# Kernel tuning notes

Measured on AMD Instinct MI355X. Metric: run time of the kernel, lower is better.

Reference implementation:

```python
import jax, jax.numpy as jnp
import numpy as np

B, SQ, SKV, D, H = 2, 2048, 2048, 1024, 16
HD = D // H  # 64
ROPE_BASE = 10000.0


def setup_inputs() -> dict:
    key = jax.random.key(0)
    ks = jax.random.split(key, 6)
    s = 1.0 / np.sqrt(D)  # keep activations well-scaled
    return {
        "x_q": jax.random.normal(ks[0], (B, SQ, D), jnp.float32),
        "x_kv": jax.random.normal(ks[1], (B, SKV, D), jnp.float32),
        "wq": jax.random.normal(ks[2], (D, D), jnp.float32) * s,
        "bq": jnp.zeros((D,), jnp.float32),
        "wk": jax.random.normal(ks[3], (D, D), jnp.float32) * s,
        "bk": jnp.zeros((D,), jnp.float32),
        "wv": jax.random.normal(ks[4], (D, D), jnp.float32) * s,
        "bv": jnp.zeros((D,), jnp.float32),
        "wo": jax.random.normal(ks[5], (D, D), jnp.float32) * s,
        "bo": jnp.zeros((D,), jnp.float32),
    }


def _rope_interleaved(x):
    # x: [B, S, H, HD]; sequential positions starting at 0 (GPT-NeoX style)
    s, hd = x.shape[1], x.shape[-1]
    dim = hd // 2
    freqs = jnp.exp(-jnp.arange(dim, dtype=x.dtype) * jnp.log(jnp.asarray(ROPE_BASE, x.dtype)) / dim)
    ang = jnp.arange(s, dtype=x.dtype)[:, None] * freqs[None, :]  # [S, dim]
    cos = jnp.cos(ang)[None, :, None, :]
    sin = jnp.sin(ang)[None, :, None, :]
    xe, xo = x[..., ::2], x[..., 1::2]
    re = xe * cos - xo * sin
    ro = xe * sin + xo * cos
    return jnp.stack([re, ro], axis=-1).reshape(x.shape)


def reference(x_q, x_kv, wq, bq, wk, bk, wv, bv, wo, bo):
    b, sq, _ = x_q.shape
    skv = x_kv.shape[1]
    q = (jnp.einsum("bsd,ed->bse", x_q, wq) + bq).reshape(b, sq, H, HD)
    k = (jnp.einsum("bsd,ed->bse", x_kv, wk) + bk).reshape(b, skv, H, HD)
    v = (jnp.einsum("bsd,ed->bse", x_kv, wv) + bv).reshape(b, skv, H, HD)
    q = _rope_interleaved(q)
    k = _rope_interleaved(k)
    scores = jnp.einsum("bqhd,bkhd->bhqk", q, k) / jnp.sqrt(jnp.asarray(HD, q.dtype))
    attn = jax.nn.softmax(scores, axis=-1)
    ctx = jnp.einsum("bhqk,bkhd->bqhd", attn, v).reshape(b, sq, D)
    return jnp.einsum("bsd,ed->bse", ctx, wo) + bo
```

## Files before the change

kernel.cpp:

```cpp
#include <hip/hip_runtime.h>
#include <cstdint>

typedef __attribute__((ext_vector_type(8))) short bf16x8;
typedef __attribute__((ext_vector_type(4))) float f32x4;
typedef __attribute__((ext_vector_type(4))) unsigned int u32x4;

#define DEV static __device__ __forceinline__

DEV unsigned short f2bf(float f) {
  unsigned int u = __builtin_bit_cast(unsigned int, f);
  u += 0x7FFFu + ((u >> 16) & 1u);
  return (unsigned short)(u >> 16);
}
#if __has_builtin(__builtin_amdgcn_cvt_pk_bf16_f32)
DEV unsigned int pkbf(float a, float b) {
  auto v = __builtin_amdgcn_cvt_pk_bf16_f32(a, b);
  return __builtin_bit_cast(unsigned int, v);
}
#else
DEV unsigned int pkbf(float a, float b) {
  return (unsigned int)f2bf(a) | ((unsigned int)f2bf(b) << 16);
}
#endif
#if __has_builtin(__builtin_amdgcn_exp2f)
#define EXP2(x) __builtin_amdgcn_exp2f(x)
#else
#define EXP2(x) exp2f(x)
#endif
DEV float bfl(unsigned int u) { return __builtin_bit_cast(float, u << 16); }
DEV float bfh(unsigned int u) { return __builtin_bit_cast(float, u & 0xFFFF0000u); }

DEV void async_copy16(const unsigned short* g, unsigned short* l) {
  __builtin_amdgcn_global_load_lds(
      (const __attribute__((address_space(1))) unsigned int*)(uintptr_t)g,
      (__attribute__((address_space(3))) unsigned int*)(uintptr_t)l,
      16, 0, 0);
}

#if __has_builtin(__builtin_amdgcn_permlane32_swap) && \
    __has_builtin(__builtin_amdgcn_permlane16_swap)
DEV void pswap(unsigned a, unsigned b, unsigned& w0, unsigned& w2, int lane) {
  (void)lane;
  auto pq = __builtin_amdgcn_permlane32_swap((int)a, (int)b, false, false);
  auto wz = __builtin_amdgcn_permlane16_swap(pq[0], pq[1], false, false);
  w0 = (unsigned)wz[0];
  w2 = (unsigned)wz[1];
}
#else
DEV void pswap(unsigned a, unsigned b, unsigned& w0, unsigned& w2, int lane) {
  int q = lane >> 4, l = lane & 15;
  int src0 = ((q & 1) << 5) + l;
  int a0 = __shfl((int)a, src0), b0 = __shfl((int)b, src0);
  int a2 = __shfl((int)a, src0 + 16), b2 = __shfl((int)b, src0 + 16);
  w0 = (unsigned)(q < 2 ? a0 : b0);
  w2 = (unsigned)(q < 2 ? a2 : b2);
}
#endif

__global__ __launch_bounds__(256) void cvt8(
    const float* __restrict__ w0, const float* __restrict__ w1,
    const float* __restrict__ w2, const float* __restrict__ w3,
    const float* __restrict__ x0, const float* __restrict__ x1,
    unsigned short* __restrict__ wsb, unsigned short* __restrict__ xb)
{
  int id = blockIdx.x * 256 + threadIdx.x;
  const float* src;
  unsigned short* dp;
  int off;
  if (id < (1 << 20)) {
    int m = id >> 18;
    off = (id & 0x3FFFF) << 2;
    src = m == 0 ? w0 : m == 1 ? w1 : m == 2 ? w2 : w3;
    dp = wsb + (((size_t)m) << 20) + off;
  } else {
    int id2 = id - (1 << 20);
    int m = id2 >> 20;
    off = (id2 & 0xFFFFF) << 2;
    src = m ? x1 : x0;
    dp = xb + (((size_t)m) << 22) + off;
  }
  float4 v = *(const float4*)(src + off);
  uint2 o;
  o.x = pkbf(v.x, v.y);
  o.y = pkbf(v.z, v.w);
  *(uint2*)dp = o;
}

__global__ __launch_bounds__(256) void gemm_qkv_bf(
    const unsigned short* __restrict__ xqb,
    const unsigned short* __restrict__ xkvb,
    const unsigned short* __restrict__ wbase,
    const float* __restrict__ bq, const float* __restrict__ bk,
    const float* __restrict__ bv,
    unsigned short* __restrict__ outq, unsigned short* __restrict__ outk,
    unsigned short* __restrict__ outvT)
{
  constexpr int K = 1024;
  __shared__ unsigned short As[2][128 * 32];
  __shared__ unsigned short Bs[2][128 * 32];
  const int z = blockIdx.z;
  const unsigned short* X = (z == 0) ? xqb : xkvb;
  const unsigned short* Wb = wbase + (((size_t)z) << 20);
  const float* bias = (z == 0) ? bq : (z == 1) ? bk : bv;

  const int tid = threadIdx.x;
  const int mBase = blockIdx.y * 128, nBase = blockIdx.x * 128;
  const int wave = tid >> 6, lane = tid & 63;
  const int quad = lane >> 4, l16 = lane & 15;
  const int wm = (wave >> 1) << 6, wn = (wave & 1) << 6;

  const int L0 = tid, L1 = 256 + tid;
  const int r0 = L0 >> 2, c0 = ((L0 & 3) ^ (r0 & 3)) << 3;
  const int r1 = L1 >> 2, c1 = ((L1 & 3) ^ (r1 & 3)) << 3;

  f32x4 acc[4][4] = {};

  async_copy16(X + (size_t)(mBase + r0) * K + c0, &As[0][L0 * 8]);
  async_copy16(X + (size_t)(mBase + r1) * K + c1, &As[0][L1 * 8]);
  async_copy16(Wb + (size_t)(nBase + r0) * K + c0, &Bs[0][L0 * 8]);
  async_copy16(Wb + (size_t)(nBase + r1) * K + c1, &Bs[0][L1 * 8]);
  __syncthreads();

  const int sw = (quad ^ (l16 & 3)) << 3;
  for (int it = 0; it < 32; ++it) {
    const int cur = it & 1;
    if (it < 31) {
      const int k0 = (it + 1) * 32;
      async_copy16(X + (size_t)(mBase + r0) * K + k0 + c0, &As[cur ^ 1][L0 * 8]);
      async_copy16(X + (size_t)(mBase + r1) * K + k0 + c1, &As[cur ^ 1][L1 * 8]);
      async_copy16(Wb + (size_t)(nBase + r0) * K + k0 + c0, &Bs[cur ^ 1][L0 * 8]);
      async_copy16(Wb + (size_t)(nBase + r1) * K + k0 + c1, &Bs[cur ^ 1][L1 * 8]);
    }
    bf16x8 af[4], bff[4];
#pragma unroll
    for (int t = 0; t < 4; ++t) {
      af[t]  = *(const bf16x8*)&As[cur][(wm + t * 16 + l16) * 32 + sw];
      bff[t] = *(const bf16x8*)&Bs[cur][(wn + t * 16 + l16) * 32 + sw];
    }
#pragma unroll
    for (int mt = 0; mt < 4; ++mt)
#pragma unroll
      for (int nt = 0; nt < 4; ++nt)
        acc[mt][nt] = __builtin_amdgcn_mfma_f32_16x16x32_bf16(af[mt], bff[nt], acc[mt][nt], 0, 0, 0);
    __syncthreads();
  }

  if (z < 2) {
    unsigned short* out = z ? outk : outq;
    const float qs = z ? 1.0f : 0.18033688011112042f;
    const int sBlk = (mBase & 2047) + wm + quad * 4;
#pragma unroll
    for (int nt = 0; nt < 4; ++nt) {
      int n = nBase + wn + nt * 16 + l16;
      float bv2 = bias[n];
      int h = n >> 6, hd = n & 63;
      int i = hd >> 1;
      int parity = n & 1;
      float f = exp2f(-(float)i * 0.4152410118609203f);
      float sf, cf;
      sincosf(f, &sf, &cf);
#pragma unroll
      for (int mt = 0; mt < 4; ++mt) {
        float ang = (float)(sBlk + mt * 16) * f;
        float s, c;
        sincosf(ang, &s, &c);
#pragma unroll
        for (int j = 0; j < 4; ++j) {
          float v = acc[mt][nt][j] + bv2;
          float pv = __shfl_xor(v, 1);
          float ce = c * qs;
          float se = (parity ? s : -s) * qs;
          float outv = v * ce + pv * se;
          int m = mBase + wm + mt * 16 + quad * 4 + j;
          int b = m >> 11, sv = m & 2047;
          out[(((size_t)(b * 16 + h) * 2048 + sv) << 6) + hd] = f2bf(outv);
          float c2 = c * cf - s * sf;
          s = s * cf + c * sf;
          c = c2;
        }
      }
    }
  } else {
#pragma unroll
    for (int nt = 0; nt < 4; ++nt) {
      int n = nBase + wn + nt * 16 + l16;
      float bv2 = bias[n];
      int h = n >> 6, hd = n & 63;
#pragma unroll
      for (int mt = 0; mt < 4; ++mt) {
        int m0 = mBase + wm + mt * 16 + quad * 4;
        int b = m0 >> 11, s = m0 & 2047;
        uint2 o;
        o.x = pkbf(acc[mt][nt][0] + bv2, acc[mt][nt][1] + bv2);
        o.y = pkbf(acc[mt][nt][2] + bv2, acc[mt][nt][3] + bv2);
        *(uint2*)&outvT[(((size_t)(b * 16 + h) * 64 + hd) << 11) + s] = o;
      }
    }
  }
}

__global__ __launch_bounds__(256) void attn_v7(
    const unsigned short* __restrict__ Qg,
    const unsigned short* __restrict__ Kg,
    const unsigned short* __restrict__ VT,
    unsigned short* __restrict__ Opart,
    float* __restrict__ lbuf)
{
  __shared__ unsigned short Ks[2][64 * 64];
  __shared__ unsigned short Vs[2][64 * 64];
  const int tid = threadIdx.x, wave = tid >> 6, lane = tid & 63;
  const int quad = lane >> 4, l16 = lane & 15;
  const int bh = blockIdx.x & 31;
  const int qt = (blockIdx.x >> 5) & 15;
  const int kvs = blockIdx.x >> 9;
  const int q0 = qt * 128 + wave * 32;
  const unsigned short* Qb = Qg + ((size_t)bh << 17);
  const unsigned short* Kb = Kg + ((size_t)bh << 17);
  const unsigned short* Vb = VT + ((size_t)bh << 17);

  const int L0 = tid, L1 = 256 + tid;
  const int r0 = L0 >> 3, r1 = L1 >> 3;
  const int c0 = ((L0 & 7) ^ (r0 & 7)) << 3;
  const int c1 = ((L1 & 7) ^ (r1 & 7)) << 3;

  bf16x8 qf[2][2];
#pragma unroll
  for (int mq = 0; mq < 2; ++mq)
#pragma unroll
    for (int kd = 0; kd < 2; ++kd)
      qf[mq][kd] = *(const bf16x8*)(Qb + (size_t)(q0 + mq * 16 + l16) * 64 + kd * 32 + quad * 8);

  f32x4 oacc[4][2] = {};
  float lacc[2] = { 0.f, 0.f };

  const int kvbeg = kvs << 10;
  const int swz = l16 & 7;

  {
    const int kv0 = kvbeg;
    async_copy16(Kb + (size_t)(kv0 + r0) * 64 + c0, &Ks[0][L0 * 8]);
    async_copy16(Kb + (size_t)(kv0 + r1) * 64 + c1, &Ks[0][L1 * 8]);
    async_copy16(Vb + (size_t)r0 * 2048 + kv0 + c0, &Vs[0][L0 * 8]);
    async_copy16(Vb + (size_t)r1 * 2048 + kv0 + c1, &Vs[0][L1 * 8]);
  }
  __syncthreads();

  for (int t = 0; t < 16; ++t) {
    const int cur = t & 1;
    if (t < 15) {
      const int kv0 = kvbeg + (t + 1) * 64;
      unsigned short* Kn = Ks[cur ^ 1];
      unsigned short* Vn = Vs[cur ^ 1];
      async_copy16(Kb + (size_t)(kv0 + r0) * 64 + c0, &Kn[L0 * 8]);
      async_copy16(Kb + (size_t)(kv0 + r1) * 64 + c1, &Kn[L1 * 8]);
      async_copy16(Vb + (size_t)r0 * 2048 + kv0 + c0, &Vn[L0 * 8]);
      async_copy16(Vb + (size_t)r1 * 2048 + kv0 + c1, &Vn[L1 * 8]);
    }
    const unsigned short* Kc = Ks[cur];
    const unsigned short* Vc = Vs[cur];

    f32x4 st[4][2] = {};
    __builtin_amdgcn_s_setprio(1);
#pragma unroll
    for (int kd = 0; kd < 2; ++kd)
#pragma unroll
      for (int tk = 0; tk < 4; ++tk) {
        bf16x8 kf = *(const bf16x8*)&Kc[(tk * 16 + l16) * 64 + (((kd * 4 + quad) ^ swz) << 3)];
#pragma unroll
        for (int mq = 0; mq < 2; ++mq)
          st[tk][mq] = __builtin_amdgcn_mfma_f32_16x16x32_bf16(kf, qf[mq][kd], st[tk][mq], 0, 0, 0);
      }
    __builtin_amdgcn_s_setprio(0);

#pragma unroll
    for (int mq = 0; mq < 2; ++mq)
#pragma unroll
      for (int tk = 0; tk < 4; ++tk)
#pragma unroll
        for (int jr = 0; jr < 4; ++jr) {
          float p = EXP2(st[tk][mq][jr]);
          st[tk][mq][jr] = p;
          lacc[mq] += p;
        }

#pragma unroll
    for (int ks = 0; ks < 2; ++ks) {
      bf16x8 pf[2];
#pragma unroll
      for (int mq = 0; mq < 2; ++mq) {
        u32x4 pw;
#pragma unroll
        for (int w = 0; w < 2; ++w) {
          unsigned a = pkbf(st[2 * ks][mq][2 * w], st[2 * ks][mq][2 * w + 1]);
          unsigned b = pkbf(st[2 * ks + 1][mq][2 * w], st[2 * ks + 1][mq][2 * w + 1]);
          unsigned w0, w2;
          pswap(a, b, w0, w2, lane);
          pw[w] = w0;
          pw[w + 2] = w2;
        }
        pf[mq] = __builtin_bit_cast(bf16x8, pw);
      }
      __builtin_amdgcn_s_setprio(1);
#pragma unroll
      for (int th = 0; th < 4; ++th) {
        bf16x8 vf = *(const bf16x8*)&Vc[(th * 16 + l16) * 64 + (((ks * 4 + quad) ^ swz) << 3)];
#pragma unroll
        for (int mq = 0; mq < 2; ++mq)
          oacc[th][mq] = __builtin_amdgcn_mfma_f32_16x16x32_bf16(vf, pf[mq], oacc[th][mq], 0, 0, 0);
      }
      __builtin_amdgcn_s_setprio(0);
    }
    __syncthreads();
  }

  const int b = bh >> 4, h = bh & 15;
  unsigned short* Od = Opart + (((size_t)kvs) << 22);
#pragma unroll
  for (int mq = 0; mq < 2; ++mq) {
    float l = lacc[mq];
    l += __shfl_xor(l, 16);
    l += __shfl_xor(l, 32);
    int s = q0 + mq * 16 + l16;
    if (quad == 0)
      lbuf[(kvs * 32 + bh) * 2048 + s] = l;
#pragma unroll
    for (int th = 0; th < 4; ++th) {
      uint2 o;
      o.x = pkbf(oacc[th][mq][0], oacc[th][mq][1]);
      o.y = pkbf(oacc[th][mq][2], oacc[th][mq][3]);
      *(uint2*)&Od[((size_t)(b * 2048 + s) << 10) + h * 64 + th * 16 + quad * 4] = o;
    }
  }
}

__global__ __launch_bounds__(256) void combine_kernel(
    const unsigned short* __restrict__ Opart, const float* __restrict__ lbuf,
    unsigned short* __restrict__ ctx)
{
  int idx = blockIdx.x * 256 + threadIdx.x;
  int m = idx >> 9;
  int c2 = idx & 511;
  int b = m >> 11, s = m & 2047;
  int h = c2 >> 5;
  int bh = b * 16 + h;
  float la = lbuf[bh * 2048 + s];
  float lb = lbuf[(32 + bh) * 2048 + s];
  float r = 1.0f / (la + lb);
  unsigned int ua = ((const unsigned int*)Opart)[idx];
  unsigned int ub = ((const unsigned int*)Opart)[(1u << 21) + idx];
  float o0 = (bfl(ua) + bfl(ub)) * r;
  float o1 = (bfh(ua) + bfh(ub)) * r;
  ((unsigned int*)ctx)[idx] = pkbf(o0, o1);
}

__global__ __launch_bounds__(256) void gemm_o_bf(
    const unsigned short* __restrict__ X,
    const unsigned short* __restrict__ Wb,
    const float* __restrict__ bias,
    float* __restrict__ out)
{
  constexpr int K = 1024;
  __shared__ unsigned short As[2][64 * 32];
  __shared__ unsigned short Bs[2][128 * 32];
  const int tid = threadIdx.x;
  const int mBase = blockIdx.y * 64, nBase = blockIdx.x * 128;
  const int wave = tid >> 6, lane = tid & 63;
  const int quad = lane >> 4, l16 = lane & 15;
  const int wm = (wave >> 1) << 5, wn = (wave & 1) << 6;

  const int La = tid, ra = La >> 2, ca = ((La & 3) ^ (ra & 3)) << 3;
  const int Lb1 = 256 + tid, rb1 = Lb1 >> 2, cb1 = ((Lb1 & 3) ^ (rb1 & 3)) << 3;

  f32x4 acc[2][4] = {};

  async_copy16(X + (size_t)(mBase + ra) * K + ca, &As[0][La * 8]);
  async_copy16(Wb + (size_t)(nBase + ra) * K + ca, &Bs[0][La * 8]);
  async_copy16(Wb + (size_t)(nBase + rb1) * K + cb1, &Bs[0][Lb1 * 8]);
  __syncthreads();

  const int sw = (quad ^ (l16 & 3)) << 3;
  for (int it = 0; it < 32; ++it) {
    const int cur = it & 1;
    if (it < 31) {
      const int k0 = (it + 1) * 32;
      async_copy16(X + (size_t)(mBase + ra) * K + k0 + ca, &As[cur ^ 1][La * 8]);
      async_copy16(Wb + (size_t)(nBase + ra) * K + k0 + ca, &Bs[cur ^ 1][La * 8]);
      async_copy16(Wb + (size_t)(nBase + rb1) * K + k0 + cb1, &Bs[cur ^ 1][Lb1 * 8]);
    }
    bf16x8 af[2], bff[4];
#pragma unroll
    for (int t = 0; t < 2; ++t)
      af[t] = *(const bf16x8*)&As[cur][(wm + t * 16 + l16) * 32 + sw];
#pragma unroll
    for (int t = 0; t < 4; ++t)
      bff[t] = *(const bf16x8*)&Bs[cur][(wn + t * 16 + l16) * 32 + sw];
#pragma unroll
    for (int mt = 0; mt < 2; ++mt)
#pragma unroll
      for (int nt = 0; nt < 4; ++nt)
        acc[mt][nt] = __builtin_amdgcn_mfma_f32_16x16x32_bf16(af[mt], bff[nt], acc[mt][nt], 0, 0, 0);
    __syncthreads();
  }

#pragma unroll
  for (int nt = 0; nt < 4; ++nt) {
    int n = nBase + wn + nt * 16 + l16;
    float bv = bias[n];
#pragma unroll
    for (int mt = 0; mt < 2; ++mt) {
#pragma unroll
      for (int j = 0; j < 4; ++j) {
        int m = mBase + wm + mt * 16 + quad * 4 + j;
        out[((size_t)m << 10) + n] = acc[mt][nt][j] + bv;
      }
    }
  }
}

extern "C" void kernel_launch(void* const* d_in, const int* in_sizes, int n_in,
                              void* d_out, int out_size, void* d_ws, size_t ws_size,
                              hipStream_t stream) {
  const float* x_q  = (const float*)d_in[0];
  const float* x_kv = (const float*)d_in[1];
  const float* wq   = (const float*)d_in[2];
  const float* bq   = (const float*)d_in[3];
  const float* wk   = (const float*)d_in[4];
  const float* bk   = (const float*)d_in[5];
  const float* wv   = (const float*)d_in[6];
  const float* bv   = (const float*)d_in[7];
  const float* wo   = (const float*)d_in[8];
  const float* bo   = (const float*)d_in[9];

  unsigned short* base = (unsigned short*)d_ws;
  unsigned short* ob   = (unsigned short*)d_out;

  unsigned short* wob  = base + (3u << 20);
  unsigned short* k    = base + (4u << 20);
  unsigned short* vT   = base + (8u << 20);
  unsigned short* q    = base + (12u << 20);
  unsigned short* ctx  = q;
  float*          lbuf = (float*)d_ws;
  unsigned short* xqb  = ob;
  unsigned short* xkvb = ob + (4u << 20);
  unsigned short* Opart = ob;
  float* out = (float*)d_out;

  cvt8<<<12288, 256, 0, stream>>>(wq, wk, wv, wo, x_q, x_kv, base, ob);
  gemm_qkv_bf<<<dim3(8, 32, 3), 256, 0, stream>>>(xqb, xkvb, base,
                                                  bq, bk, bv, q, k, vT);
  attn_v7<<<1024, 256, 0, stream>>>(q, k, vT, Opart, lbuf);
  combine_kernel<<<8192, 256, 0, stream>>>(Opart, lbuf, ctx);
  gemm_o_bf<<<dim3(8, 64), 256, 0, stream>>>(ctx, wob, bo, out);
}
```

Baseline: 240.8 us.

## Software-pipeline PV matmul one tile behind QK and compute row sums via MFMA

The attention loop now issues the P·V MFMAs for the previous KV tile before computing QK^T for the current tile. This lets matrix work overlap with the exp and packing of probabilities. V gets a triple-buffered LDS ring so the lagging tile stays resident while the next tile loads. The softmax denominator is now computed by an MFMA against a ones vector on the bf16-rounded probabilities, replacing scalar adds and shuffles. The cost is more LDS and registers, and row sums that now come from bf16 values.

```diff
diff --git a/kernel.cpp b/kernel.cpp
--- a/kernel.cpp
+++ b/kernel.cpp
@@ -199,7 +199,7 @@
   }
 }
 
-__global__ __launch_bounds__(256) void attn_v7(
+__global__ __launch_bounds__(256) void attn_v8(
     const unsigned short* __restrict__ Qg,
     const unsigned short* __restrict__ Kg,
     const unsigned short* __restrict__ VT,
@@ -207,7 +207,7 @@
     float* __restrict__ lbuf)
 {
   __shared__ unsigned short Ks[2][64 * 64];
-  __shared__ unsigned short Vs[2][64 * 64];
+  __shared__ unsigned short Vs[3][64 * 64];
   const int tid = threadIdx.x, wave = tid >> 6, lane = tid & 63;
   const int quad = lane >> 4, l16 = lane & 15;
   const int bh = blockIdx.x & 31;
@@ -230,35 +230,55 @@
     for (int kd = 0; kd < 2; ++kd)
       qf[mq][kd] = *(const bf16x8*)(Qb + (size_t)(q0 + mq * 16 + l16) * 64 + kd * 32 + quad * 8);
 
+  bf16x8 onesf;
+#pragma unroll
+  for (int i = 0; i < 8; ++i) onesf[i] = (short)0x3F80;
+
   f32x4 oacc[4][2] = {};
-  float lacc[2] = { 0.f, 0.f };
+  f32x4 laccv[2] = {};
+  bf16x8 pfp[2][2];
 
   const int kvbeg = kvs << 10;
   const int swz = l16 & 7;
 
-  {
-    const int kv0 = kvbeg;
-    async_copy16(Kb + (size_t)(kv0 + r0) * 64 + c0, &Ks[0][L0 * 8]);
-    async_copy16(Kb + (size_t)(kv0 + r1) * 64 + c1, &Ks[0][L1 * 8]);
-    async_copy16(Vb + (size_t)r0 * 2048 + kv0 + c0, &Vs[0][L0 * 8]);
-    async_copy16(Vb + (size_t)r1 * 2048 + kv0 + c1, &Vs[0][L1 * 8]);
-  }
+  async_copy16(Kb + (size_t)(kvbeg + r0) * 64 + c0, &Ks[0][L0 * 8]);
+  async_copy16(Kb + (size_t)(kvbeg + r1) * 64 + c1, &Ks[0][L1 * 8]);
+  async_copy16(Vb + (size_t)r0 * 2048 + kvbeg + c0, &Vs[0][L0 * 8]);
+  async_copy16(Vb + (size_t)r1 * 2048 + kvbeg + c1, &Vs[0][L1 * 8]);
   __syncthreads();
 
   for (int t = 0; t < 16; ++t) {
-    const int cur = t & 1;
+    const int kcur = t & 1;
     if (t < 15) {
       const int kv0 = kvbeg + (t + 1) * 64;
-      unsigned short* Kn = Ks[cur ^ 1];
-      unsigned short* Vn = Vs[cur ^ 1];
+      unsigned short* Kn = Ks[kcur ^ 1];
+      unsigned short* Vn = Vs[(t + 1) % 3];
       async_copy16(Kb + (size_t)(kv0 + r0) * 64 + c0, &Kn[L0 * 8]);
       async_copy16(Kb + (size_t)(kv0 + r1) * 64 + c1, &Kn[L1 * 8]);
       async_copy16(Vb + (size_t)r0 * 2048 + kv0 + c0, &Vn[L0 * 8]);
       async_copy16(Vb + (size_t)r1 * 2048 + kv0 + c1, &Vn[L1 * 8]);
     }
-    const unsigned short* Kc = Ks[cur];
-    const unsigned short* Vc = Vs[cur];
-
+
+    if (t > 0) {
+      const unsigned short* Vp = Vs[(t - 1) % 3];
+      __builtin_amdgcn_s_setprio(1);
+#pragma unroll
+      for (int ks = 0; ks < 2; ++ks) {
+#pragma unroll
+        for (int th = 0; th < 4; ++th) {
+          bf16x8 vf = *(const bf16x8*)&Vp[(th * 16 + l16) * 64 + (((ks * 4 + quad) ^ swz) << 3)];
+#pragma unroll
+          for (int mq = 0; mq < 2; ++mq)
+            oacc[th][mq] = __builtin_amdgcn_mfma_f32_16x16x32_bf16(vf, pfp[ks][mq], oacc[th][mq], 0, 0, 0);
+        }
+#pragma unroll
+        for (int mq = 0; mq < 2; ++mq)
+          laccv[mq] = __builtin_amdgcn_mfma_f32_16x16x32_bf16(onesf, pfp[ks][mq], laccv[mq], 0, 0, 0);
+      }
+      __builtin_amdgcn_s_setprio(0);
+    }
+
+    const unsigned short* Kc = Ks[kcur];
     f32x4 st[4][2] = {};
     __builtin_amdgcn_s_setprio(1);
 #pragma unroll
@@ -277,15 +297,11 @@
 #pragma unroll
       for (int tk = 0; tk < 4; ++tk)
 #pragma unroll
-        for (int jr = 0; jr < 4; ++jr) {
-          float p = EXP2(st[tk][mq][jr]);
-          st[tk][mq][jr] = p;
-          lacc[mq] += p;
-        }
-
-#pragma unroll
-    for (int ks = 0; ks < 2; ++ks) {
-      bf16x8 pf[2];
+        for (int jr = 0; jr < 4; ++jr)
+          st[tk][mq][jr] = EXP2(st[tk][mq][jr]);
+
+#pragma unroll
+    for (int ks = 0; ks < 2; ++ks)
 #pragma unroll
       for (int mq = 0; mq < 2; ++mq) {
         u32x4 pw;
@@ -298,31 +314,38 @@
           pw[w] = w0;
           pw[w + 2] = w2;
         }
-        pf[mq] = __builtin_bit_cast(bf16x8, pw);
-      }
-      __builtin_amdgcn_s_setprio(1);
+        pfp[ks][mq] = __builtin_bit_cast(bf16x8, pw);
+      }
+
+    __syncthreads();
+  }
+
+  {
+    const unsigned short* Vp = Vs[15 % 3];
+    __builtin_amdgcn_s_setprio(1);
+#pragma unroll
+    for (int ks = 0; ks < 2; ++ks) {
 #pragma unroll
       for (int th = 0; th < 4; ++th) {
-        bf16x8 vf = *(const bf16x8*)&Vc[(th * 16 + l16) * 64 + (((ks * 4 + quad) ^ swz) << 3)];
+        bf16x8 vf = *(const bf16x8*)&Vp[(th * 16 + l16) * 64 + (((ks * 4 + quad) ^ swz) << 3)];
 #pragma unroll
         for (int mq = 0; mq < 2; ++mq)
-          oacc[th][mq] = __builtin_amdgcn_mfma_f32_16x16x32_bf16(vf, pf[mq], oacc[th][mq], 0, 0, 0);
-      }
-      __builtin_amdgcn_s_setprio(0);
-    }
-    __syncthreads();
+          oacc[th][mq] = __builtin_amdgcn_mfma_f32_16x16x32_bf16(vf, pfp[ks][mq], oacc[th][mq], 0, 0, 0);
+      }
+#pragma unroll
+      for (int mq = 0; mq < 2; ++mq)
+        laccv[mq] = __builtin_amdgcn_mfma_f32_16x16x32_bf16(onesf, pfp[ks][mq], laccv[mq], 0, 0, 0);
+    }
+    __builtin_amdgcn_s_setprio(0);
   }
 
   const int b = bh >> 4, h = bh & 15;
   unsigned short* Od = Opart + (((size_t)kvs) << 22);
 #pragma unroll
   for (int mq = 0; mq < 2; ++mq) {
-    float l = lacc[mq];
-    l += __shfl_xor(l, 16);
-    l += __shfl_xor(l, 32);
     int s = q0 + mq * 16 + l16;
     if (quad == 0)
-      lbuf[(kvs * 32 + bh) * 2048 + s] = l;
+      lbuf[(kvs * 32 + bh) * 2048 + s] = laccv[mq][0];
 #pragma unroll
     for (int th = 0; th < 4; ++th) {
       uint2 o;
@@ -448,7 +471,7 @@
   cvt8<<<12288, 256, 0, stream>>>(wq, wk, wv, wo, x_q, x_kv, base, ob);
   gemm_qkv_bf<<<dim3(8, 32, 3), 256, 0, stream>>>(xqb, xkvb, base,
                                                   bq, bk, bv, q, k, vT);
-  attn_v7<<<1024, 256, 0, stream>>>(q, k, vT, Opart, lbuf);
+  attn_v8<<<1024, 256, 0, stream>>>(q, k, vT, Opart, lbuf);
   combine_kernel<<<8192, 256, 0, stream>>>(Opart, lbuf, ctx);
   gemm_o_bf<<<dim3(8, 64), 256, 0, stream>>>(ctx, wob, bo, out);
 }
```

After: 233.7 us. 2.9% less time.
